# Optimization experiments

Measured on AMD Instinct MI355X. Metric: run time of the kernel, lower is better.

Reference implementation:

```python
import jax, jax.numpy as jnp
import numpy as np

B, S, DIM = 2, 2048, 2048
H = 16
Q_LORA, KV_LORA = 512, 512
D_NOPE, D_ROPE, D_V = 128, 64, 128
D_QK = D_NOPE + D_ROPE  # 192
SCALE = D_QK ** -0.5
EPS = 1e-6


def rmsnorm(x, w):
    return x * jax.lax.rsqrt(jnp.mean(x * x, axis=-1, keepdims=True) + EPS) * w


def apply_rope(x, cos, sin):
    # x: [B, S, h, d] with d even; cos/sin: [S, d//2] (complex-pair rotation)
    xs = x.reshape(*x.shape[:-1], -1, 2)
    x0, x1 = xs[..., 0], xs[..., 1]
    c = cos[None, :, None, :]
    s = sin[None, :, None, :]
    out = jnp.stack([x0 * c - x1 * s, x0 * s + x1 * c], axis=-1)
    return out.reshape(x.shape)


def setup_inputs() -> dict:
    key = jax.random.key(0)
    ks = jax.random.split(key, 8)
    std = 0.02
    x = jax.random.normal(ks[0], (B, S, DIM), dtype=jnp.float32)
    wq_a_w = jax.random.normal(ks[1], (DIM, Q_LORA), dtype=jnp.float32) * std
    wq_a_b = jnp.zeros((Q_LORA,), dtype=jnp.float32)
    q_norm_w = jnp.ones((Q_LORA,), dtype=jnp.float32)
    wq_b_w = jax.random.normal(ks[2], (Q_LORA, H * D_QK), dtype=jnp.float32) * std
    wkv_a_w = jax.random.normal(ks[3], (DIM, KV_LORA + D_ROPE), dtype=jnp.float32) * std
    wkv_a_b = jnp.zeros((KV_LORA + D_ROPE,), dtype=jnp.float32)
    kv_norm_w = jnp.ones((KV_LORA,), dtype=jnp.float32)
    wkv_b_w = jax.random.normal(ks[4], (KV_LORA, H * (D_NOPE + D_V)), dtype=jnp.float32) * std
    wo_w = jax.random.normal(ks[5], (H * D_V, DIM), dtype=jnp.float32) * std
    # rotary table: freqs_cis[t, i] = exp(1j * t * 10000^{-2i/d})
    inv_freq = 1.0 / (10000.0 ** (np.arange(0, D_ROPE, 2, dtype=np.float32) / D_ROPE))
    t = np.arange(S, dtype=np.float32)
    ang = np.outer(t, inv_freq)  # [S, D_ROPE//2]
    freqs_cos = jnp.asarray(np.cos(ang), dtype=jnp.float32)
    freqs_sin = jnp.asarray(np.sin(ang), dtype=jnp.float32)
    # causal mask (prefill): 0 on/below diagonal, -1e9 above
    mask = jnp.where(jnp.arange(S)[:, None] >= jnp.arange(S)[None, :], 0.0, -1e9).astype(jnp.float32)
    return {"x": x, "wq_a_w": wq_a_w, "wq_a_b": wq_a_b, "q_norm_w": q_norm_w,
            "wq_b_w": wq_b_w, "wkv_a_w": wkv_a_w, "wkv_a_b": wkv_a_b,
            "kv_norm_w": kv_norm_w, "wkv_b_w": wkv_b_w, "wo_w": wo_w,
            "freqs_cos": freqs_cos, "freqs_sin": freqs_sin, "mask": mask,
            "start_pos": 0}


def reference(x, wq_a_w, wq_a_b, q_norm_w, wq_b_w, wkv_a_w, wkv_a_b,
              kv_norm_w, wkv_b_w, wo_w, freqs_cos, freqs_sin, mask, start_pos):
    bsz, seqlen, _ = x.shape
    # low-rank Q: wq_b(q_norm(wq_a(x)))
    q = rmsnorm(x @ wq_a_w + wq_a_b, q_norm_w) @ wq_b_w
    q = q.reshape(bsz, seqlen, H, D_QK)
    q_nope, q_pe = q[..., :D_NOPE], q[..., D_NOPE:]
    q_pe = apply_rope(q_pe, freqs_cos, freqs_sin)
    # low-rank KV
    kv_full = x @ wkv_a_w + wkv_a_b
    kv, k_pe = kv_full[..., :KV_LORA], kv_full[..., KV_LORA:]
    k_pe = apply_rope(k_pe[:, :, None, :], freqs_cos, freqs_sin)  # [B,S,1,D_ROPE]
    kv = rmsnorm(kv, kv_norm_w) @ wkv_b_w
    kv = kv.reshape(bsz, seqlen, H, D_NOPE + D_V)
    k_nope, v = kv[..., :D_NOPE], kv[..., D_NOPE:]
    k = jnp.concatenate([k_nope, jnp.broadcast_to(k_pe, (bsz, seqlen, H, D_ROPE))], axis=-1)
    # prefill (start_pos=0): cache[:, :end_pos] == freshly written k, v
    q = jnp.concatenate([q_nope, q_pe], axis=-1)
    scores = jnp.einsum('bshd,bthd->bsht', q, k) * SCALE
    scores = scores + mask[None, :, None, :]
    attn = jax.nn.softmax(scores.astype(jnp.float32), axis=-1).astype(q.dtype)
    out = jnp.einsum('bsht,bthd->bshd', attn, v)
    return out.reshape(bsz, seqlen, H * D_V) @ wo_w
```

## Files before the change

kernel.cpp:

```cpp
#include <hip/hip_runtime.h>
#include <hip/hip_bf16.h>

typedef unsigned short u16;
typedef unsigned int u32;
typedef __attribute__((ext_vector_type(8))) __bf16 bf16x8;
typedef __attribute__((ext_vector_type(4))) float f32x4;
typedef __attribute__((ext_vector_type(4))) u32 u32x4;

#define S_LEN 2048
#define BF16_ONE 0x3F80u

__device__ __forceinline__ float b2f(u16 u) {
  union { unsigned u; float f; } v; v.u = ((unsigned)u) << 16; return v.f;
}
__device__ __forceinline__ u16 f2b(float f) {
  union { float f; unsigned u; } v; v.f = f;
  unsigned r = v.u + 0x7fffu + ((v.u >> 16) & 1u);
  return (u16)(r >> 16);
}

__device__ __forceinline__ void glds16(const u16* g, u16* l) {
  __builtin_amdgcn_global_load_lds((const __attribute__((address_space(1))) void*)g,
                                   (__attribute__((address_space(3))) void*)l, 16, 0, 0);
}

__device__ __forceinline__ bool probe_f32(const u16* p) { return p[0] != (u16)BF16_ONE; }

struct CvtDesc {
  const void* src[7];
  u16* dst[7];
  int cum[8];
};
__global__ __launch_bounds__(256) void cvt_batch(CvtDesc d, const u16* __restrict__ probe,
                                                 int total) {
  int i = blockIdx.x * 256 + threadIdx.x;
  if (i >= total) return;
  int t = 0;
#pragma unroll
  for (int k = 1; k < 7; ++k) t += (i >= d.cum[k]);
  int li = i - d.cum[t];
  if (probe_f32(probe)) {
    const float* s = (const float*)d.src[t] + (long)li * 8;
    u16 tmp[8];
#pragma unroll
    for (int j = 0; j < 8; ++j) tmp[j] = f2b(s[j]);
    *(u32x4*)(d.dst[t] + (long)li * 8) = *(const u32x4*)tmp;
  } else {
    *(u32x4*)(d.dst[t] + (long)li * 8) = ((const u32x4*)d.src[t])[li];
  }
}

struct TrDesc {
  const void* in[5];
  u16* out[5];
  int R[5], C[5];
  int tcum[6];
  float scale[5];
};
__global__ __launch_bounds__(256) void transpose_batch(TrDesc d,
                                                       const u16* __restrict__ probe) {
  __shared__ u16 tile[32][33];
  int bid = blockIdx.x;
  int t = 0;
#pragma unroll
  for (int k = 1; k < 5; ++k) t += (bid >= d.tcum[k]);
  int rem = bid - d.tcum[t];
  const int R = d.R[t], C = d.C[t];
  const int tilesX = C >> 5;
  const int bx = rem % tilesX, by = rem / tilesX;
  const int c0 = bx * 32, r0 = by * 32;
  const int tx = threadIdx.x, ty = threadIdx.y;
  const float sc = d.scale[t];
  if (probe_f32(probe)) {
    const float* inf = (const float*)d.in[t];
#pragma unroll
    for (int i = 0; i < 4; ++i)
      tile[ty + i * 8][tx] = f2b(inf[(long)(r0 + ty + i * 8) * C + c0 + tx] * sc);
  } else {
    const u16* inb = (const u16*)d.in[t];
#pragma unroll
    for (int i = 0; i < 4; ++i)
      tile[ty + i * 8][tx] = f2b(b2f(inb[(long)(r0 + ty + i * 8) * C + c0 + tx]) * sc);
  }
  __syncthreads();
  u16* outp = d.out[t];
#pragma unroll
  for (int i = 0; i < 4; ++i)
    outp[(long)(c0 + ty + i * 8) * R + r0 + tx] = tile[tx][ty + i * 8];
}

__global__ __launch_bounds__(256) void transpose_v(const u16* __restrict__ kvb,
                                                   u16* __restrict__ vt) {
  __shared__ u16 tile[32][33];
  int s0 = blockIdx.x * 32, d0 = blockIdx.y * 32, bh = blockIdx.z;
  int b = bh >> 4, h = bh & 15;
  int tx = threadIdx.x, ty = threadIdx.y;
#pragma unroll
  for (int i = 0; i < 4; ++i)
    tile[ty + i * 8][tx] =
        kvb[((long)b * S_LEN + s0 + ty + i * 8) * 4096 + h * 256 + 128 + d0 + tx];
  __syncthreads();
#pragma unroll
  for (int i = 0; i < 4; ++i)
    vt[((long)bh * 128 + d0 + ty + i * 8) * S_LEN + s0 + tx] = tile[tx][ty + i * 8];
}

template <int MT>
__global__ __launch_bounds__(256) void gemm_bt(const u16* __restrict__ A,
                                               const u16* __restrict__ Bt,
                                               const u16* __restrict__ bias,
                                               void* __restrict__ Cv,
                                               int M, int N, int K,
                                               const u16* __restrict__ oprobe) {
  constexpr int MI = MT / 32;
  __shared__ u16 As[2][MT * 32];
  __shared__ u16 Bs[2][128 * 32];
  const int tid = threadIdx.x;
  const int lane = tid & 63;
  const int w = tid >> 6;
  const int quad = lane >> 4;
  const int l16 = lane & 15;
  const int m0 = blockIdx.y * MT;
  const int n0 = blockIdx.x * 128;
  const int wm = (w >> 1) * (MT / 2);
  const int wn = (w & 1) * 64;

  const f32x4 zero = {0.f, 0.f, 0.f, 0.f};
  f32x4 acc[MI][4];
#pragma unroll
  for (int i = 0; i < MI; ++i)
#pragma unroll
    for (int j = 0; j < 4; ++j) acc[i][j] = zero;

  auto stage = [&](int k0, int buf) {
#pragma unroll
    for (int cc = 0; cc < MT * 4; cc += 256) {
      int j = cc + tid, ar = j >> 2, ak = ((j & 3) ^ (ar & 3)) * 8;
      glds16(A + (long)(m0 + ar) * K + k0 + ak, As[buf] + j * 8);
    }
#pragma unroll
    for (int cc = 0; cc < 512; cc += 256) {
      int j = cc + tid, br = j >> 2, bk = ((j & 3) ^ (br & 3)) * 8;
      int bn = n0 + br; if (bn > N - 1) bn = N - 1;
      glds16(Bt + (long)bn * K + k0 + bk, Bs[buf] + j * 8);
    }
  };

  const int nk = K >> 5;
  stage(0, 0);
  for (int t = 0; t < nk; ++t) {
    __syncthreads();
    if (t + 1 < nk) stage((t + 1) << 5, (t + 1) & 1);
    const u16* as = As[t & 1];
    const u16* bs = Bs[t & 1];
    bf16x8 af[MI], bfr[4];
#pragma unroll
    for (int mi = 0; mi < MI; ++mi)
      af[mi] = *(const bf16x8*)(as + (wm + mi * 16 + l16) * 32 +
                                ((quad ^ (l16 & 3)) * 8));
#pragma unroll
    for (int ni = 0; ni < 4; ++ni)
      bfr[ni] = *(const bf16x8*)(bs + (wn + ni * 16 + l16) * 32 +
                                 ((quad ^ (l16 & 3)) * 8));
#pragma unroll
    for (int mi = 0; mi < MI; ++mi)
#pragma unroll
      for (int ni = 0; ni < 4; ++ni)
        acc[mi][ni] = __builtin_amdgcn_mfma_f32_16x16x32_bf16(af[mi], bfr[ni],
                                                              acc[mi][ni], 0, 0, 0);
  }

  u16* C = (u16*)Cv;
  float* Cf = (float*)Cv;
  const bool of32 = oprobe && probe_f32(oprobe);
#pragma unroll
  for (int ni = 0; ni < 4; ++ni) {
    int col = n0 + wn + ni * 16 + l16;
    if (col >= N) continue;
    float bv = bias ? b2f(bias[col]) : 0.0f;
#pragma unroll
    for (int mi = 0; mi < MI; ++mi) {
      int row = m0 + wm + mi * 16 + quad * 4;
#pragma unroll
      for (int r = 0; r < 4; ++r) {
        float val = acc[mi][ni][r] + bv;
        if (of32) Cf[(long)(row + r) * N + col] = val;
        else      C[(long)(row + r) * N + col] = f2b(val);
      }
    }
  }
}

__global__ __launch_bounds__(256) void rmsnorm512(const u16* __restrict__ in, int in_stride,
                                                  const u16* __restrict__ w,
                                                  u16* __restrict__ out, int out_stride) {
  __shared__ float red[4];
  int row = blockIdx.x, tid = threadIdx.x;
  const u16* x = in + (long)row * in_stride;
  float v0 = b2f(x[tid]), v1 = b2f(x[tid + 256]);
  float ss = v0 * v0 + v1 * v1;
#pragma unroll
  for (int off = 1; off < 64; off <<= 1) ss += __shfl_xor(ss, off);
  if ((tid & 63) == 0) red[tid >> 6] = ss;
  __syncthreads();
  float tot = red[0] + red[1] + red[2] + red[3];
  float r = rsqrtf(tot * (1.0f / 512.0f) + 1e-6f);
  u16* y = out + (long)row * out_stride;
  y[tid] = f2b(v0 * r * b2f(w[tid]));
  y[tid + 256] = f2b(v1 * r * b2f(w[tid + 256]));
}

__global__ __launch_bounds__(256) void rope_q_kernel(u16* __restrict__ q,
                                                     const u16* __restrict__ fc,
                                                     const u16* __restrict__ fs) {
  int i = blockIdx.x * 256 + threadIdx.x;
  int pair = i & 31;
  int h = (i >> 5) & 15;
  int row = i >> 9;
  int pos = row & (S_LEN - 1);
  long base = (long)row * 3072 + h * 192 + 128 + pair * 2;
  float x0 = b2f(q[base]), x1 = b2f(q[base + 1]);
  float c = b2f(fc[pos * 32 + pair]), s = b2f(fs[pos * 32 + pair]);
  q[base] = f2b(x0 * c - x1 * s);
  q[base + 1] = f2b(x0 * s + x1 * c);
}

__global__ __launch_bounds__(256) void rope_k_kernel(const u16* __restrict__ kva,
                                                     u16* __restrict__ kpe,
                                                     const u16* __restrict__ fc,
                                                     const u16* __restrict__ fs) {
  int i = blockIdx.x * 256 + threadIdx.x;
  int pair = i & 31;
  int row = i >> 5;
  int pos = row & (S_LEN - 1);
  long sb = (long)row * 576 + 512 + pair * 2;
  float x0 = b2f(kva[sb]), x1 = b2f(kva[sb + 1]);
  float c = b2f(fc[pos * 32 + pair]), s = b2f(fs[pos * 32 + pair]);
  kpe[(long)row * 64 + pair * 2] = f2b(x0 * c - x1 * s);
  kpe[(long)row * 64 + pair * 2 + 1] = f2b(x0 * s + x1 * c);
}

__global__ __launch_bounds__(512, 1) void mla_attn(const u16* __restrict__ q,
                                                   const u16* __restrict__ kvb,
                                                   const u16* __restrict__ vt,
                                                   const u16* __restrict__ kpe,
                                                   u16* __restrict__ o) {
  __shared__ u16 Ks[2][64 * 192];
  __shared__ u16 Vts[2][128 * 64];
  __shared__ u16 Ps[8][16 * 72];
  const int tid = threadIdx.x;
  const int w = tid >> 6;
  const int lane = tid & 63;
  const int quad = lane >> 4;
  const int l16 = lane & 15;
  const int bh = blockIdx.x;
  const int b = bh >> 4, h = bh & 15;
  const long rowbase = (long)b * S_LEN;
  const f32x4 zero = {0.f, 0.f, 0.f, 0.f};

  auto stage_k = [&](int t0s, u16* dst) {
#pragma unroll
    for (int tt = 0; tt < 3; ++tt) {
      int j = tt * 512 + tid;
      int r = j / 24, csw = j % 24;
      int c = csw ^ (r & 7);
      const u16* src = (c < 16)
                           ? (kvb + (rowbase + t0s + r) * 4096 + h * 256 + c * 8)
                           : (kpe + (rowbase + t0s + r) * 64 + (c - 16) * 8);
      glds16(src, dst + j * 8);
    }
  };
  auto stage_v = [&](int t0s, u16* dst) {
#pragma unroll
    for (int tt = 0; tt < 2; ++tt) {
      int j = tt * 512 + tid;
      int d = j >> 3, c = (j & 7) ^ (d & 7);
      glds16(vt + ((long)bh * 128 + d) * S_LEN + t0s + c * 8, dst + j * 8);
    }
  };

  for (int pass = 0; pass < 2; ++pass) {
    const int jt = pass ? (15 - (int)blockIdx.y) : (int)blockIdx.y;
    const int q0 = jt * 128;
    const int ntiles = 2 * jt + 2;
    const int rowlo = q0 + w * 16;

    const u16* qrow_p = q + (rowbase + q0 + w * 16 + l16) * 3072 + h * 192;
    bf16x8 qf[6];
#pragma unroll
    for (int kk = 0; kk < 6; ++kk)
      qf[kk] = *(const bf16x8*)(qrow_p + kk * 32 + quad * 8);

    float m_r[4] = {-INFINITY, -INFINITY, -INFINITY, -INFINITY};
    float l_r[4] = {0.f, 0.f, 0.f, 0.f};
    f32x4 oacc[8];
#pragma unroll
    for (int i = 0; i < 8; ++i) oacc[i] = zero;

    __syncthreads();
    stage_k(0, Ks[0]);
    stage_v(0, Vts[0]);

    for (int t = 0; t < ntiles; ++t) {
      __syncthreads();
      if (t + 1 < ntiles) {
        stage_k((t + 1) * 64, Ks[(t + 1) & 1]);
        stage_v((t + 1) * 64, Vts[(t + 1) & 1]);
      }
      const int t0 = t * 64;
      if (rowlo + 15 < t0) continue;
      const u16* ks = Ks[t & 1];
      const u16* vs = Vts[t & 1];
      const bool needmask = (t0 + 63 > rowlo);

      f32x4 s[4] = {zero, zero, zero, zero};
#pragma unroll
      for (int kk = 0; kk < 6; ++kk) {
        const int csw = ((kk * 4 + quad) ^ (l16 & 7)) * 8;
#pragma unroll
        for (int g = 0; g < 4; ++g) {
          bf16x8 kf = *(const bf16x8*)(ks + (g * 16 + l16) * 192 + csw);
          s[g] = __builtin_amdgcn_mfma_f32_16x16x32_bf16(qf[kk], kf, s[g], 0, 0, 0);
        }
      }

      const int qrow = rowlo + quad * 4;
      float al[4];
      u16* pw = Ps[w];
#pragma unroll
      for (int r = 0; r < 4; ++r) {
        float a0 = s[0][r], a1 = s[1][r], a2 = s[2][r], a3 = s[3][r];
        if (needmask) {
          int rr = qrow + r;
          if (t0 + l16 > rr)      a0 = -1e30f;
          if (t0 + 16 + l16 > rr) a1 = -1e30f;
          if (t0 + 32 + l16 > rr) a2 = -1e30f;
          if (t0 + 48 + l16 > rr) a3 = -1e30f;
        }
        float v = fmaxf(fmaxf(a0, a1), fmaxf(a2, a3));
        v = fmaxf(v, __shfl_xor(v, 1, 16));
        v = fmaxf(v, __shfl_xor(v, 2, 16));
        v = fmaxf(v, __shfl_xor(v, 4, 16));
        v = fmaxf(v, __shfl_xor(v, 8, 16));
        float mnew = fmaxf(m_r[r], v);
        float alpha = __expf(m_r[r] - mnew);
        float e0 = __expf(a0 - mnew);
        float e1 = __expf(a1 - mnew);
        float e2 = __expf(a2 - mnew);
        float e3 = __expf(a3 - mnew);
        l_r[r] = l_r[r] * alpha + ((e0 + e1) + (e2 + e3));
        m_r[r] = mnew;
        al[r] = alpha;
        int rb = (quad * 4 + r) * 72;
        pw[rb + l16] = f2b(e0);
        pw[rb + 16 + l16] = f2b(e1);
        pw[rb + 32 + l16] = f2b(e2);
        pw[rb + 48 + l16] = f2b(e3);
      }
      __asm__ __volatile__("" ::: "memory");
#pragma unroll
      for (int nt = 0; nt < 8; ++nt) {
        f32x4 tt = oacc[nt];
        tt[0] *= al[0]; tt[1] *= al[1]; tt[2] *= al[2]; tt[3] *= al[3];
        oacc[nt] = tt;
      }
      bf16x8 ap0 = *(const bf16x8*)(pw + l16 * 72 + quad * 8);
      bf16x8 ap1 = *(const bf16x8*)(pw + l16 * 72 + 32 + quad * 8);
#pragma unroll
      for (int nt = 0; nt < 8; ++nt) {
        bf16x8 bv0 = *(const bf16x8*)(vs + (nt * 16 + l16) * 64 +
                                      ((quad ^ (l16 & 7)) * 8));
        bf16x8 bv1 = *(const bf16x8*)(vs + (nt * 16 + l16) * 64 +
                                      (((4 + quad) ^ (l16 & 7)) * 8));
        oacc[nt] = __builtin_amdgcn_mfma_f32_16x16x32_bf16(ap0, bv0, oacc[nt], 0, 0, 0);
        oacc[nt] = __builtin_amdgcn_mfma_f32_16x16x32_bf16(ap1, bv1, oacc[nt], 0, 0, 0);
      }
    }

#pragma unroll
    for (int r = 0; r < 4; ++r) {
      float ls = l_r[r];
      ls += __shfl_xor(ls, 1, 16);
      ls += __shfl_xor(ls, 2, 16);
      ls += __shfl_xor(ls, 4, 16);
      ls += __shfl_xor(ls, 8, 16);
      l_r[r] = ls;
    }
    const long orow = rowbase + q0 + w * 16 + quad * 4;
#pragma unroll
    for (int nt = 0; nt < 8; ++nt)
#pragma unroll
      for (int r = 0; r < 4; ++r)
        o[(orow + r) * 2048 + h * 128 + nt * 16 + l16] = f2b(oacc[nt][r] / l_r[r]);
  }
}

extern "C" void kernel_launch(void* const* d_in, const int* in_sizes, int n_in,
                              void* d_out, int out_size, void* d_ws, size_t ws_size,
                              hipStream_t stream) {
  const void* x_raw    = d_in[0];
  const void* wqa_raw  = d_in[1];
  const void* wqab_raw = d_in[2];
  const void* qnw_raw  = d_in[3];
  const void* wqb_raw  = d_in[4];
  const void* wkva_raw = d_in[5];
  const void* wkvab_raw= d_in[6];
  const void* kvnw_raw = d_in[7];
  const void* wkvb_raw = d_in[8];
  const void* wo_raw   = d_in[9];
  const void* fc_raw   = d_in[10];
  const void* fs_raw   = d_in[11];
  const u16* probe = (const u16*)qnw_raw;
  const float SC = 0.07216878364870323f;

  char* ws = (char*)d_ws;
  size_t off = 0;
  auto alloc = [&](size_t n) { void* p = ws + off; off += (n + 255) & ~(size_t)255; return p; };
  u16* xb     = (u16*)alloc(4096ull * 2048 * 2);
  u16* fcb    = (u16*)alloc(2048ull * 32 * 2);
  u16* fsb    = (u16*)alloc(2048ull * 32 * 2);
  u16* wqab_b = (u16*)alloc(512ull * 2);
  u16* qnw_b  = (u16*)alloc(512ull * 2);
  u16* wkvab_b= (u16*)alloc(576ull * 2);
  u16* kvnw_b = (u16*)alloc(512ull * 2);
  u16* wqa_t  = (u16*)alloc(512ull * 2048 * 2);
  u16* wqb_t  = (u16*)alloc(3072ull * 512 * 2);
  u16* wkva_t = (u16*)alloc(576ull * 2048 * 2);
  u16* wkvb_t = (u16*)alloc(4096ull * 512 * 2);
  u16* wo_t   = (u16*)alloc(2048ull * 2048 * 2);
  u16* qa     = (u16*)alloc(4096ull * 512 * 2);
  u16* qbuf   = (u16*)alloc(4096ull * 3072 * 2);
  u16* kva    = (u16*)alloc(4096ull * 576 * 2);
  u16* kvn    = (u16*)alloc(4096ull * 512 * 2);
  u16* kpe    = (u16*)alloc(4096ull * 64 * 2);
  u16* kvb    = (u16*)alloc(4096ull * 4096 * 2);
  u16* vtb    = (u16*)alloc(32ull * 128 * 2048 * 2);
  u16* attn   = (u16*)alloc(4096ull * 2048 * 2);

  CvtDesc cd;
  const void* csrc[7] = {x_raw, fc_raw, fs_raw, wqab_raw, qnw_raw, wkvab_raw, kvnw_raw};
  u16* cdst[7] = {xb, fcb, fsb, wqab_b, qnw_b, wkvab_b, kvnw_b};
  long cn[7] = {4096l * 2048, 2048l * 32, 2048l * 32, 512, 512, 576, 512};
  int cum = 0;
  for (int i = 0; i < 7; ++i) {
    cd.src[i] = csrc[i]; cd.dst[i] = cdst[i];
    cd.cum[i] = cum; cum += (int)(cn[i] / 8);
  }
  cd.cum[7] = cum;
  cvt_batch<<<(cum + 255) / 256, 256, 0, stream>>>(cd, probe, cum);

  TrDesc td;
  const void* tin[5] = {wqa_raw, wqb_raw, wkva_raw, wkvb_raw, wo_raw};
  u16* tout[5] = {wqa_t, wqb_t, wkva_t, wkvb_t, wo_t};
  int tR[5] = {2048, 512, 2048, 512, 2048};
  int tC[5] = {512, 3072, 576, 4096, 2048};
  float tsc[5] = {1.0f, SC, 1.0f, 1.0f, 1.0f};
  int tcum = 0;
  for (int i = 0; i < 5; ++i) {
    td.in[i] = tin[i]; td.out[i] = tout[i];
    td.R[i] = tR[i]; td.C[i] = tC[i]; td.scale[i] = tsc[i];
    td.tcum[i] = tcum; tcum += (tR[i] / 32) * (tC[i] / 32);
  }
  td.tcum[5] = tcum;
  transpose_batch<<<tcum, dim3(32, 8), 0, stream>>>(td, probe);

  gemm_bt<64><<<dim3(4, 64), 256, 0, stream>>>(xb, wqa_t, wqab_b, qa, 4096, 512, 2048, nullptr);
  rmsnorm512<<<4096, 256, 0, stream>>>(qa, 512, qnw_b, qa, 512);
  gemm_bt<128><<<dim3(24, 32), 256, 0, stream>>>(qa, wqb_t, nullptr, qbuf, 4096, 3072, 512, nullptr);
  rope_q_kernel<<<8192, 256, 0, stream>>>(qbuf, fcb, fsb);

  gemm_bt<64><<<dim3(5, 64), 256, 0, stream>>>(xb, wkva_t, wkvab_b, kva, 4096, 576, 2048, nullptr);
  rmsnorm512<<<4096, 256, 0, stream>>>(kva, 576, kvnw_b, kvn, 512);
  rope_k_kernel<<<512, 256, 0, stream>>>(kva, kpe, fcb, fsb);
  gemm_bt<128><<<dim3(32, 32), 256, 0, stream>>>(kvn, wkvb_t, nullptr, kvb, 4096, 4096, 512, nullptr);
  transpose_v<<<dim3(64, 4, 32), dim3(32, 8), 0, stream>>>(kvb, vtb);

  mla_attn<<<dim3(32, 8), 512, 0, stream>>>(qbuf, kvb, vtb, kpe, attn);

  gemm_bt<128><<<dim3(16, 32), 256, 0, stream>>>(attn, wo_t, nullptr, d_out, 4096, 2048, 2048, probe);
}
```

Baseline: 452.7 us.

## Transpose QK MFMA so softmax is lane-local, add lazy rescale and packed bf16 stores

The QK^T MFMA operands are swapped so each lane holds one query row's scores. Row max and sum then need only two cross-lane shuffles instead of per-row 16-lane reductions. The online-softmax rescale of the output accumulator is skipped unless the row max grows by more than 8, which removes most alpha multiplies and exps. P is written to LDS with packed v_cvt_pk_bf16 stores, and s_setprio is raised around the MFMA blocks. Skipping the rescale lets exponentials grow by up to e^8 relative to the stored max, which slightly changes bf16 rounding of P.

```diff
diff --git a/kernel.cpp b/kernel.cpp
--- a/kernel.cpp
+++ b/kernel.cpp
@@ -6,6 +6,7 @@
 typedef __attribute__((ext_vector_type(8))) __bf16 bf16x8;
 typedef __attribute__((ext_vector_type(4))) float f32x4;
 typedef __attribute__((ext_vector_type(4))) u32 u32x4;
+typedef __attribute__((ext_vector_type(2))) u32 u32x2;
 
 #define S_LEN 2048
 #define BF16_ONE 0x3F80u
@@ -17,6 +18,11 @@
   union { float f; unsigned u; } v; v.f = f;
   unsigned r = v.u + 0x7fffu + ((v.u >> 16) & 1u);
   return (u16)(r >> 16);
+}
+__device__ __forceinline__ u32 cvt_pk_bf16(float a, float b) {
+  u32 r;
+  asm("v_cvt_pk_bf16_f32 %0, %1, %2" : "=v"(r) : "v"(a), "v"(b));
+  return r;
 }
 
 __device__ __forceinline__ void glds16(const u16* g, u16* l) {
@@ -285,14 +291,14 @@
     const int ntiles = 2 * jt + 2;
     const int rowlo = q0 + w * 16;
 
-    const u16* qrow_p = q + (rowbase + q0 + w * 16 + l16) * 3072 + h * 192;
+    const u16* qrow_p = q + (rowbase + rowlo + l16) * 3072 + h * 192;
     bf16x8 qf[6];
 #pragma unroll
     for (int kk = 0; kk < 6; ++kk)
       qf[kk] = *(const bf16x8*)(qrow_p + kk * 32 + quad * 8);
 
-    float m_r[4] = {-INFINITY, -INFINITY, -INFINITY, -INFINITY};
-    float l_r[4] = {0.f, 0.f, 0.f, 0.f};
+    float m_r = -INFINITY;
+    float l_r = 0.f;
     f32x4 oacc[8];
 #pragma unroll
     for (int i = 0; i < 8; ++i) oacc[i] = zero;
@@ -314,58 +320,72 @@
       const bool needmask = (t0 + 63 > rowlo);
 
       f32x4 s[4] = {zero, zero, zero, zero};
+      __builtin_amdgcn_s_setprio(1);
 #pragma unroll
       for (int kk = 0; kk < 6; ++kk) {
         const int csw = ((kk * 4 + quad) ^ (l16 & 7)) * 8;
 #pragma unroll
         for (int g = 0; g < 4; ++g) {
           bf16x8 kf = *(const bf16x8*)(ks + (g * 16 + l16) * 192 + csw);
-          s[g] = __builtin_amdgcn_mfma_f32_16x16x32_bf16(qf[kk], kf, s[g], 0, 0, 0);
+          s[g] = __builtin_amdgcn_mfma_f32_16x16x32_bf16(kf, qf[kk], s[g], 0, 0, 0);
         }
       }
-
-      const int qrow = rowlo + quad * 4;
-      float al[4];
+      __builtin_amdgcn_s_setprio(0);
+
+      if (needmask) {
+        const int lim = rowlo + l16 - t0 - quad * 4;
+#pragma unroll
+        for (int g = 0; g < 4; ++g)
+#pragma unroll
+          for (int r = 0; r < 4; ++r)
+            s[g][r] = (g * 16 + r > lim) ? -1e30f : s[g][r];
+      }
+
+      float mx0 = fmaxf(fmaxf(s[0][0], s[0][1]), fmaxf(s[0][2], s[0][3]));
+      float mx1 = fmaxf(fmaxf(s[1][0], s[1][1]), fmaxf(s[1][2], s[1][3]));
+      float mx2 = fmaxf(fmaxf(s[2][0], s[2][1]), fmaxf(s[2][2], s[2][3]));
+      float mx3 = fmaxf(fmaxf(s[3][0], s[3][1]), fmaxf(s[3][2], s[3][3]));
+      float vmax = fmaxf(fmaxf(mx0, mx1), fmaxf(mx2, mx3));
+      vmax = fmaxf(vmax, __shfl_xor(vmax, 16));
+      vmax = fmaxf(vmax, __shfl_xor(vmax, 32));
+
+      if (!__all(vmax <= m_r + 8.0f)) {
+        float mnew = fmaxf(m_r, vmax);
+        float alpha = __expf(m_r - mnew);
+        m_r = mnew;
+        l_r *= alpha;
+        float al0 = __shfl(alpha, (lane & 48) | (quad * 4 + 0));
+        float al1 = __shfl(alpha, (lane & 48) | (quad * 4 + 1));
+        float al2 = __shfl(alpha, (lane & 48) | (quad * 4 + 2));
+        float al3 = __shfl(alpha, (lane & 48) | (quad * 4 + 3));
+#pragma unroll
+        for (int nt = 0; nt < 8; ++nt) {
+          f32x4 tt = oacc[nt];
+          tt[0] *= al0; tt[1] *= al1; tt[2] *= al2; tt[3] *= al3;
+          oacc[nt] = tt;
+        }
+      }
+
       u16* pw = Ps[w];
-#pragma unroll
-      for (int r = 0; r < 4; ++r) {
-        float a0 = s[0][r], a1 = s[1][r], a2 = s[2][r], a3 = s[3][r];
-        if (needmask) {
-          int rr = qrow + r;
-          if (t0 + l16 > rr)      a0 = -1e30f;
-          if (t0 + 16 + l16 > rr) a1 = -1e30f;
-          if (t0 + 32 + l16 > rr) a2 = -1e30f;
-          if (t0 + 48 + l16 > rr) a3 = -1e30f;
-        }
-        float v = fmaxf(fmaxf(a0, a1), fmaxf(a2, a3));
-        v = fmaxf(v, __shfl_xor(v, 1, 16));
-        v = fmaxf(v, __shfl_xor(v, 2, 16));
-        v = fmaxf(v, __shfl_xor(v, 4, 16));
-        v = fmaxf(v, __shfl_xor(v, 8, 16));
-        float mnew = fmaxf(m_r[r], v);
-        float alpha = __expf(m_r[r] - mnew);
-        float e0 = __expf(a0 - mnew);
-        float e1 = __expf(a1 - mnew);
-        float e2 = __expf(a2 - mnew);
-        float e3 = __expf(a3 - mnew);
-        l_r[r] = l_r[r] * alpha + ((e0 + e1) + (e2 + e3));
-        m_r[r] = mnew;
-        al[r] = alpha;
-        int rb = (quad * 4 + r) * 72;
-        pw[rb + l16] = f2b(e0);
-        pw[rb + 16 + l16] = f2b(e1);
-        pw[rb + 32 + l16] = f2b(e2);
-        pw[rb + 48 + l16] = f2b(e3);
-      }
+      float sum = 0.f;
+#pragma unroll
+      for (int g = 0; g < 4; ++g) {
+        float e0 = __expf(s[g][0] - m_r);
+        float e1 = __expf(s[g][1] - m_r);
+        float e2 = __expf(s[g][2] - m_r);
+        float e3 = __expf(s[g][3] - m_r);
+        sum += (e0 + e1) + (e2 + e3);
+        u32x2 pk;
+        pk.x = cvt_pk_bf16(e0, e1);
+        pk.y = cvt_pk_bf16(e2, e3);
+        *(u32x2*)(pw + l16 * 72 + g * 16 + quad * 4) = pk;
+      }
+      l_r += sum;
+
       __asm__ __volatile__("" ::: "memory");
-#pragma unroll
-      for (int nt = 0; nt < 8; ++nt) {
-        f32x4 tt = oacc[nt];
-        tt[0] *= al[0]; tt[1] *= al[1]; tt[2] *= al[2]; tt[3] *= al[3];
-        oacc[nt] = tt;
-      }
       bf16x8 ap0 = *(const bf16x8*)(pw + l16 * 72 + quad * 8);
       bf16x8 ap1 = *(const bf16x8*)(pw + l16 * 72 + 32 + quad * 8);
+      __builtin_amdgcn_s_setprio(1);
 #pragma unroll
       for (int nt = 0; nt < 8; ++nt) {
         bf16x8 bv0 = *(const bf16x8*)(vs + (nt * 16 + l16) * 64 +
@@ -375,23 +395,24 @@
         oacc[nt] = __builtin_amdgcn_mfma_f32_16x16x32_bf16(ap0, bv0, oacc[nt], 0, 0, 0);
         oacc[nt] = __builtin_amdgcn_mfma_f32_16x16x32_bf16(ap1, bv1, oacc[nt], 0, 0, 0);
       }
-    }
-
-#pragma unroll
-    for (int r = 0; r < 4; ++r) {
-      float ls = l_r[r];
-      ls += __shfl_xor(ls, 1, 16);
-      ls += __shfl_xor(ls, 2, 16);
-      ls += __shfl_xor(ls, 4, 16);
-      ls += __shfl_xor(ls, 8, 16);
-      l_r[r] = ls;
-    }
+      __builtin_amdgcn_s_setprio(0);
+    }
+
+    float ls = l_r;
+    ls += __shfl_xor(ls, 16);
+    ls += __shfl_xor(ls, 32);
+    float i0 = __fdividef(1.0f, __shfl(ls, (lane & 48) | (quad * 4 + 0)));
+    float i1 = __fdividef(1.0f, __shfl(ls, (lane & 48) | (quad * 4 + 1)));
+    float i2 = __fdividef(1.0f, __shfl(ls, (lane & 48) | (quad * 4 + 2)));
+    float i3 = __fdividef(1.0f, __shfl(ls, (lane & 48) | (quad * 4 + 3)));
     const long orow = rowbase + q0 + w * 16 + quad * 4;
 #pragma unroll
-    for (int nt = 0; nt < 8; ++nt)
-#pragma unroll
-      for (int r = 0; r < 4; ++r)
-        o[(orow + r) * 2048 + h * 128 + nt * 16 + l16] = f2b(oacc[nt][r] / l_r[r]);
+    for (int nt = 0; nt < 8; ++nt) {
+      o[(orow + 0) * 2048 + h * 128 + nt * 16 + l16] = f2b(oacc[nt][0] * i0);
+      o[(orow + 1) * 2048 + h * 128 + nt * 16 + l16] = f2b(oacc[nt][1] * i1);
+      o[(orow + 2) * 2048 + h * 128 + nt * 16 + l16] = f2b(oacc[nt][2] * i2);
+      o[(orow + 3) * 2048 + h * 128 + nt * 16 + l16] = f2b(oacc[nt][3] * i3);
+    }
   }
 }
 
```

Result: faster. 427.7 us (-5.5%).
